# Kernel optimization log

Measured on AMD Instinct MI355X. Metric: run time of the kernel, lower is better.

## Reference

```python
import jax, jax.numpy as jnp
import numpy as np

T = 2048        # tokens
HID = 4096      # hidden_size
H = 32          # num attention heads
KV = 8          # num key/value heads (GQA)
D = HID // H    # head_dim = 128
THETA = 10000.0


def setup_inputs() -> dict:
    key = jax.random.key(0)
    k1, k2, k3 = jax.random.split(key, 3)
    hidden_states = jax.random.normal(k1, (T, HID), jnp.float32)
    positions = jnp.arange(T, dtype=jnp.int32)
    Wqkv = jax.random.normal(k2, ((H + 2 * KV) * D, HID), jnp.float32) * 0.02
    Wo = jax.random.normal(k3, (HID, H * D), jnp.float32) * 0.02
    return {"hidden_states": hidden_states, "positions": positions,
            "Wqkv": Wqkv, "Wo": Wo}


def _rope(positions, x):
    """Neox-style rotary embedding. x: [T, h, D], positions: [T]."""
    half = D // 2
    inv_freq = 1.0 / (THETA ** (jnp.arange(half, dtype=jnp.float32) / half))
    ang = positions.astype(jnp.float32)[:, None] * inv_freq      # [T, half]
    cos = jnp.cos(ang)[:, None, :]                                # [T, 1, half]
    sin = jnp.sin(ang)[:, None, :]
    x1, x2 = x[..., :half], x[..., half:]
    return jnp.concatenate([x1 * cos - x2 * sin, x2 * cos + x1 * sin], axis=-1)


def reference(hidden_states, positions, Wqkv, Wo):
    # fused QKV projection (no bias)
    qkv = hidden_states @ Wqkv.T                                  # [T, (H+2KV)*D]
    q, k, v = jnp.split(qkv, [H * D, H * D + KV * D], axis=1)
    q = q.reshape(T, H, D)
    k = k.reshape(T, KV, D)
    v = v.reshape(T, KV, D)
    # RoPE on q and k
    q = _rope(positions, q)
    k = _rope(positions, k)
    # GQA: expand kv heads to match q heads
    g = H // KV
    k = jnp.repeat(k, g, axis=1)                                  # [T, H, D]
    v = jnp.repeat(v, g, axis=1)
    # causal attention (flash-attention math)
    scores = jnp.einsum('thd,shd->hts', q, k) * (D ** -0.5)       # [H, T, T]
    causal = jnp.tril(jnp.ones((T, T), dtype=bool))
    scores = jnp.where(causal[None], scores, jnp.float32(-1e30))
    probs = jax.nn.softmax(scores, axis=-1)
    attn = jnp.einsum('hts,shd->thd', probs, v).reshape(T, H * D)
    # output projection
    return attn @ Wo.T
```

## Files before the change

### kernel.cpp

```cpp
#include <hip/hip_runtime.h>
#include <stdint.h>

#define T_SEQ 2048
#define HIDDEN 4096
#define NHEAD 32
#define NKV 8
#define HDIM 128
#define QKVN 6144

typedef __bf16 bf16x8 __attribute__((ext_vector_type(8)));
typedef float f32x4 __attribute__((ext_vector_type(4)));
typedef unsigned short u16;
typedef u16 u16x8 __attribute__((ext_vector_type(8)));
typedef u16 u16x4 __attribute__((ext_vector_type(4)));

__device__ __forceinline__ u16 f2bf(float f) {
  uint32_t u = __builtin_bit_cast(uint32_t, f);
  u = (u + 0x7fffu + ((u >> 16) & 1u)) >> 16;
  return (u16)u;
}
__device__ __forceinline__ float bf2f(u16 h) {
  uint32_t u = ((uint32_t)h) << 16;
  return __builtin_bit_cast(float, u);
}

__device__ __forceinline__ void gload16(const void* g, void* l) {
  __builtin_amdgcn_global_load_lds(
      (__attribute__((address_space(1))) void*)(uintptr_t)g,
      (__attribute__((address_space(3))) void*)(uintptr_t)l, 16, 0, 0);
}

__global__ void cvt_f32_bf16(const float* __restrict__ in, u16* __restrict__ out, int n) {
  int i = (blockIdx.x * blockDim.x + threadIdx.x) * 4;
  int stride = gridDim.x * blockDim.x * 4;
  for (; i < n; i += stride) {
    float4 v = *(const float4*)(in + i);
    u16x4 o;
    o.x = f2bf(v.x); o.y = f2bf(v.y); o.z = f2bf(v.z); o.w = f2bf(v.w);
    *(u16x4*)(out + i) = o;
  }
}

__global__ void rope_kernel(u16* __restrict__ qkv, const int* __restrict__ pos) {
  int idx = blockIdx.x * blockDim.x + threadIdx.x;
  if (idx >= T_SEQ * 40 * 64) return;
  int i = idx & 63;
  int head = (idx >> 6) % 40;
  int t = idx / (40 * 64);
  int base = head < NHEAD ? head * HDIM : NHEAD * HDIM + (head - NHEAD) * HDIM;
  float p = (float)pos[t];
  float inv_freq = exp2f(-(float)i * (13.287712379549449f / 64.0f));
  float ang = p * inv_freq;
  float s, c;
  sincosf(ang, &s, &c);
  u16* p1 = qkv + (size_t)t * QKVN + base + i;
  u16* p2 = p1 + 64;
  float x1 = bf2f(*p1), x2 = bf2f(*p2);
  *p1 = f2bf(x1 * c - x2 * s);
  *p2 = f2bf(x2 * c + x1 * s);
}

__device__ __forceinline__ void storeC(float* p, float v) { *p = v; }
__device__ __forceinline__ void storeC(u16* p, float v) { *p = f2bf(v); }
__device__ __forceinline__ f32x4 mfma16(bf16x8 a, bf16x8 b, f32x4 c) {
  return __builtin_amdgcn_mfma_f32_16x16x32_bf16(a, b, c, 0, 0, 0);
}

template <typename OutT, bool FUSED>
__global__ void __launch_bounds__(512, 2)
gemm256(const u16* __restrict__ A, const u16* __restrict__ B,
        OutT* __restrict__ C0, OutT* __restrict__ C1,
        int N, int K, int NT, int sliceBlocks, int nGemm,
        int nbx, int rw, int rh,
        const float* __restrict__ cvt_in, u16* __restrict__ cvt_out, int cvt_n4) {
  if (FUSED && (int)blockIdx.x >= nGemm) {
    int i = (blockIdx.x - nGemm) * blockDim.x + threadIdx.x;
    int stride = (gridDim.x - nGemm) * blockDim.x;
    for (; i < cvt_n4; i += stride) {
      float4 v = ((const float4*)cvt_in)[i];
      u16x4 o;
      o.x = f2bf(v.x); o.y = f2bf(v.y); o.z = f2bf(v.z); o.w = f2bf(v.w);
      ((u16x4*)cvt_out)[i] = o;
    }
    return;
  }

  __shared__ u16 As_[2][256 * 64];
  __shared__ u16 Bs_[2][256 * 64];

  const int tid = threadIdx.x;
  const int lane = tid & 63;
  const int w = tid >> 6;
  const int wr = w >> 2, wc = w & 3;
  const int l15 = lane & 15, lg = lane >> 4;

  const int bid = blockIdx.x;
  const int slice = bid / sliceBlocks;
  const int wi = bid % sliceBlocks;
  const int k0 = slice * (NT << 6);
  OutT* __restrict__ C = slice ? C1 : C0;

  const int c8 = wi & 7, i8 = wi >> 3;
  const int rpr = nbx / rw;
  const int by = (c8 / rpr) * rh + (i8 % rh);
  const int bx = (c8 % rpr) * rw + (i8 / rh);
  const int bm = by * 256, bn = bx * 256;

  const int u_lo = w * 64 + lane, u_hi = u_lo + 512;
  const int r0 = u_lo >> 3, s0 = (u_lo & 7) ^ (r0 & 7);
  const int r1 = u_hi >> 3, s1 = (u_hi & 7) ^ (r1 & 7);
  const u16* a0s0 = A + (size_t)(bm + r0) * K + k0 + s0 * 8;
  const u16* a0s1 = A + (size_t)(bm + r1) * K + k0 + s1 * 8;
  const u16* a1s0 = A + (size_t)(bm + 128 + r0) * K + k0 + s0 * 8;
  const u16* a1s1 = A + (size_t)(bm + 128 + r1) * K + k0 + s1 * 8;
  const u16* b0s0 = B + (size_t)(bn + r0) * K + k0 + s0 * 8;
  const u16* b0s1 = B + (size_t)(bn + r1) * K + k0 + s1 * 8;
  const u16* b1s0 = B + (size_t)(bn + 128 + r0) * K + k0 + s0 * 8;
  const u16* b1s1 = B + (size_t)(bn + 128 + r1) * K + k0 + s1 * 8;

  const int ax = l15 & 7;
  const int sl0 = (lg ^ ax) * 8;
  const int sl1 = ((4 + lg) ^ ax) * 8;
  const int a_row = (wr * 128 + l15) * 64;
  const int b_row = (wc * 64 + l15) * 64;

  f32x4 acc[8][4] = {};
  bf16x8 bfr[4][2];

#define BARRIER() asm volatile("s_barrier" ::: "memory")
#define WAITBAR(n_) asm volatile("s_waitcnt vmcnt(" #n_ ")\n\ts_barrier" ::: "memory")
#define STAGE_HALF(p0_, p1_, dst_, t_)                                         \
  {                                                                            \
    gload16((p0_) + (size_t)(t_) * 64, (dst_) + (size_t)w * 512);              \
    gload16((p1_) + (size_t)(t_) * 64, (dst_) + 4096 + (size_t)w * 512);       \
  }

  STAGE_HALF(a0s0, a0s1, &As_[0][0], 0);
  STAGE_HALF(a1s0, a1s1, &As_[0][8192], 0);
  STAGE_HALF(b0s0, b0s1, &Bs_[0][0], 0);
  STAGE_HALF(b1s0, b1s1, &Bs_[0][8192], 0);
  STAGE_HALF(b0s0, b0s1, &Bs_[1][0], 1);
  STAGE_HALF(b1s0, b1s1, &Bs_[1][8192], 1);
  WAITBAR(4);

  for (int v = 0; v < NT; ++v) {
    const int cur = v & 1, alt = cur ^ 1;
    const u16* Ac = &As_[cur][0];
    const u16* Bc = &Bs_[cur][0];
    const bool s1ok = (v + 1) < NT, s2ok = (v + 2) < NT;

#define MFMA_QUAD(p_, A0_, A1_, A2_, A3_)                                      \
    __builtin_amdgcn_s_setprio(1);                                             \
    _Pragma("unroll") for (int ni = 0; ni < 4; ++ni) {                         \
      acc[2 * (p_)][ni] = mfma16(A0_, bfr[ni][0], acc[2 * (p_)][ni]);          \
      acc[2 * (p_)][ni] = mfma16(A1_, bfr[ni][1], acc[2 * (p_)][ni]);          \
      acc[2 * (p_) + 1][ni] = mfma16(A2_, bfr[ni][0], acc[2 * (p_) + 1][ni]);  \
      acc[2 * (p_) + 1][ni] = mfma16(A3_, bfr[ni][1], acc[2 * (p_) + 1][ni]);  \
    }                                                                          \
    __builtin_amdgcn_s_setprio(0);

    {
#pragma unroll
      for (int ni = 0; ni < 4; ++ni) {
        bfr[ni][0] = *(const bf16x8*)&Bc[b_row + ni * 1024 + sl0];
        bfr[ni][1] = *(const bf16x8*)&Bc[b_row + ni * 1024 + sl1];
      }
      bf16x8 f0 = *(const bf16x8*)&Ac[a_row + 0 * 1024 + sl0];
      bf16x8 f1 = *(const bf16x8*)&Ac[a_row + 0 * 1024 + sl1];
      bf16x8 f2 = *(const bf16x8*)&Ac[a_row + 1 * 1024 + sl0];
      bf16x8 f3 = *(const bf16x8*)&Ac[a_row + 1 * 1024 + sl1];
      if (s1ok) STAGE_HALF(a0s0, a0s1, &As_[alt][0], v + 1);
      BARRIER();
      MFMA_QUAD(0, f0, f1, f2, f3);
      BARRIER();
    }
    {
      bf16x8 f0 = *(const bf16x8*)&Ac[a_row + 2 * 1024 + sl0];
      bf16x8 f1 = *(const bf16x8*)&Ac[a_row + 2 * 1024 + sl1];
      bf16x8 f2 = *(const bf16x8*)&Ac[a_row + 3 * 1024 + sl0];
      bf16x8 f3 = *(const bf16x8*)&Ac[a_row + 3 * 1024 + sl1];
      if (s1ok) STAGE_HALF(a1s0, a1s1, &As_[alt][8192], v + 1);
      if (s2ok) STAGE_HALF(b0s0, b0s1, &Bs_[cur][0], v + 2);
      BARRIER();
      MFMA_QUAD(1, f0, f1, f2, f3);
      BARRIER();
    }
    {
      bf16x8 f0 = *(const bf16x8*)&Ac[a_row + 4 * 1024 + sl0];
      bf16x8 f1 = *(const bf16x8*)&Ac[a_row + 4 * 1024 + sl1];
      bf16x8 f2 = *(const bf16x8*)&Ac[a_row + 5 * 1024 + sl0];
      bf16x8 f3 = *(const bf16x8*)&Ac[a_row + 5 * 1024 + sl1];
      if (s2ok) STAGE_HALF(b1s0, b1s1, &Bs_[cur][8192], v + 2);
      BARRIER();
      MFMA_QUAD(2, f0, f1, f2, f3);
      BARRIER();
    }
    {
      bf16x8 f0 = *(const bf16x8*)&Ac[a_row + 6 * 1024 + sl0];
      bf16x8 f1 = *(const bf16x8*)&Ac[a_row + 6 * 1024 + sl1];
      bf16x8 f2 = *(const bf16x8*)&Ac[a_row + 7 * 1024 + sl0];
      bf16x8 f3 = *(const bf16x8*)&Ac[a_row + 7 * 1024 + sl1];
      BARRIER();
      MFMA_QUAD(3, f0, f1, f2, f3);
      if (s2ok) { WAITBAR(4); } else { WAITBAR(0); }
    }
#undef MFMA_QUAD
  }

#pragma unroll
  for (int mi = 0; mi < 8; ++mi)
#pragma unroll
    for (int ni = 0; ni < 4; ++ni)
#pragma unroll
      for (int r = 0; r < 4; ++r) {
        int row = bm + wr * 128 + mi * 16 + lg * 4 + r;
        int col = bn + wc * 64 + ni * 16 + l15;
        storeC(&C[(size_t)row * N + col], acc[mi][ni][r]);
      }
#undef STAGE_HALF
#undef WAITBAR
#undef BARRIER
}

__global__ void reduce_add(float* __restrict__ out, const float* __restrict__ part, int n4) {
  int i = blockIdx.x * blockDim.x + threadIdx.x;
  int stride = gridDim.x * blockDim.x;
  for (; i < n4; i += stride) {
    float4 a = ((const float4*)out)[i];
    float4 b = ((const float4*)part)[i];
    a.x += b.x; a.y += b.y; a.z += b.z; a.w += b.w;
    ((float4*)out)[i] = a;
  }
}

__global__ void __launch_bounds__(256)
attn_kernel(const u16* __restrict__ qkv, u16* __restrict__ out) {
  __shared__ u16 Ksh[2][64 * 128];
  __shared__ u16 Vsh[2][128 * 64];
  __shared__ u16 Psh[4][16 * 64];

  const int tid = threadIdx.x;
  const int lane = tid & 63;
  const int w = tid >> 6;
  const int l15 = lane & 15, lg = lane >> 4;

  const int bid = blockIdx.x;
  const int kvh = bid & 7;
  const int hg = (bid >> 3) & 3;
  const int qi = 31 - (bid >> 5);
  const int h = kvh * 4 + hg;
  const int q0 = qi * 64;
  const int nt = qi + 1;

  const u16* Kg = qkv + NHEAD * HDIM + kvh * HDIM;
  const u16* Vg = qkv + (NHEAD + NKV) * HDIM + kvh * HDIM;

  bf16x8 qa[4];
  {
    const u16* qrow = qkv + (size_t)(q0 + w * 16 + l15) * QKVN + h * HDIM + lg * 8;
#pragma unroll
    for (int ks = 0; ks < 4; ++ks) qa[ks] = *(const bf16x8*)(qrow + ks * 32);
  }

  f32x4 acc_o[8] = {};
  float m[4], lsum[4];
#pragma unroll
  for (int r = 0; r < 4; ++r) { m[r] = -1e30f; lsum[r] = 0.f; }

  const float scale = 0.088388347648318447f;

#define STAGE_K(kv0, p)                                                        \
  {                                                                            \
    _Pragma("unroll") for (int rnd = 0; rnd < 4; ++rnd) {                      \
      int cc = rnd * 256 + tid;                                                \
      int krow = cc >> 4, kslot = cc & 15;                                     \
      gload16(Kg + (size_t)((kv0) + krow) * QKVN + (kslot ^ (krow & 7)) * 8,   \
              &Ksh[p][(rnd * 256 + w * 64) * 8]);                              \
    }                                                                          \
  }
#define LOAD_V(kv0, vr)                                                        \
  {                                                                            \
    _Pragma("unroll") for (int rnd = 0; rnd < 4; ++rnd) {                      \
      int cc = rnd * 256 + tid;                                                \
      int vrow = cc >> 4, d0 = (cc & 15) * 8;                                  \
      vr[rnd] = *(const u16x8*)(Vg + (size_t)((kv0) + vrow) * QKVN + d0);      \
    }                                                                          \
  }
#define WRITE_V(vr, p)                                                         \
  {                                                                            \
    _Pragma("unroll") for (int rnd = 0; rnd < 4; ++rnd) {                      \
      int cc = rnd * 256 + tid;                                                \
      int vrow = cc >> 4, d0 = (cc & 15) * 8;                                  \
      _Pragma("unroll") for (int j = 0; j < 8; ++j) {                          \
        int d = d0 + j;                                                        \
        Vsh[p][d * 64 + (((vrow >> 3) ^ (d & 7) ^ ((d >> 3) & 7)) * 8) +       \
               (vrow & 7)] = vr[rnd][j];                                       \
      }                                                                        \
    }                                                                          \
  }

  u16x8 vreg[4];
  STAGE_K(0, 0);
  LOAD_V(0, vreg);
  WRITE_V(vreg, 0);
  __syncthreads();

  for (int t = 0; t < nt; ++t) {
    const int p = t & 1;
    const int kv0 = t * 64;
    const bool more = (t + 1 < nt);
    u16x8 vnext[4];
    if (more) {
      STAGE_K(kv0 + 64, p ^ 1);
      LOAD_V(kv0 + 64, vnext);
    }

    f32x4 s[4] = {};
#pragma unroll
    for (int ks = 0; ks < 4; ++ks) {
#pragma unroll
      for (int n = 0; n < 4; ++n) {
        int row16 = n * 16 + l15;
        bf16x8 kf = *(const bf16x8*)&Ksh[p][row16 * 128 +
                                            (((ks * 4 + lg) ^ (row16 & 7)) * 8)];
        s[n] = __builtin_amdgcn_mfma_f32_16x16x32_bf16(qa[ks], kf, s[n], 0, 0, 0);
      }
    }

    const bool diag = (t == nt - 1);
    float alpha[4];
#pragma unroll
    for (int r = 0; r < 4; ++r) {
      int tq = q0 + w * 16 + lg * 4 + r;
      float mx = -1e30f;
#pragma unroll
      for (int n = 0; n < 4; ++n) {
        float v = s[n][r] * scale;
        if (diag && (kv0 + n * 16 + l15) > tq) v = -1e30f;
        s[n][r] = v;
        mx = fmaxf(mx, v);
      }
#pragma unroll
      for (int msk = 1; msk < 16; msk <<= 1) mx = fmaxf(mx, __shfl_xor(mx, msk, 64));
      float mn = fmaxf(m[r], mx);
      alpha[r] = __expf(m[r] - mn);
      m[r] = mn;
      float ps = 0.f;
#pragma unroll
      for (int n = 0; n < 4; ++n) {
        float pv = __expf(s[n][r] - mn);
        s[n][r] = pv;
        ps += pv;
      }
#pragma unroll
      for (int msk = 1; msk < 16; msk <<= 1) ps += __shfl_xor(ps, msk, 64);
      lsum[r] = lsum[r] * alpha[r] + ps;
      int prow = lg * 4 + r;
#pragma unroll
      for (int n = 0; n < 4; ++n)
        Psh[w][prow * 64 + (((n * 2 + (l15 >> 3)) ^ (prow & 7)) * 8) + (l15 & 7)] =
            f2bf(s[n][r]);
    }
#pragma unroll
    for (int f = 0; f < 8; ++f)
#pragma unroll
      for (int r = 0; r < 4; ++r) acc_o[f][r] *= alpha[r];

#pragma unroll
    for (int ks = 0; ks < 2; ++ks) {
      bf16x8 pa = *(const bf16x8*)&Psh[w][l15 * 64 + (((ks * 4 + lg) ^ (l15 & 7)) * 8)];
#pragma unroll
      for (int nd = 0; nd < 8; ++nd) {
        int d = nd * 16 + l15;
        bf16x8 bv = *(const bf16x8*)&Vsh[p][d * 64 +
                        (((ks * 4 + lg) ^ (d & 7) ^ ((d >> 3) & 7)) * 8)];
        acc_o[nd] = __builtin_amdgcn_mfma_f32_16x16x32_bf16(pa, bv, acc_o[nd], 0, 0, 0);
      }
    }

    if (more) WRITE_V(vnext, p ^ 1);
    __syncthreads();
  }

#pragma unroll
  for (int nd = 0; nd < 8; ++nd)
#pragma unroll
    for (int r = 0; r < 4; ++r) {
      int row = q0 + w * 16 + lg * 4 + r;
      int col = h * HDIM + nd * 16 + l15;
      out[(size_t)row * (NHEAD * HDIM) + col] = f2bf(acc_o[nd][r] / lsum[r]);
    }
#undef STAGE_K
#undef LOAD_V
#undef WRITE_V
}

extern "C" void kernel_launch(void* const* d_in, const int* in_sizes, int n_in,
                              void* d_out, int out_size, void* d_ws, size_t ws_size,
                              hipStream_t stream) {
  const float* hs   = (const float*)d_in[0];
  const int*   pos  = (const int*)d_in[1];
  const float* wqkv = (const float*)d_in[2];
  const float* wo   = (const float*)d_in[3];
  float* out = (float*)d_out;
  uint8_t* ws = (uint8_t*)d_ws;

  if (ws_size < 142606336u) return;
  u16* hs_bf   = (u16*)(ws + 0);
  u16* wqkv_bf = (u16*)(ws + 16777216u);
  u16* wo_bf   = (u16*)(ws + 67108864u);
  u16* qkv_bf  = (u16*)(ws + 100663296u);
  u16* attn_bf = (u16*)(ws + 125829120u);
  float* part  = (float*)(ws + 16777216u);

  cvt_f32_bf16<<<2048, 256, 0, stream>>>(hs, hs_bf, T_SEQ * HIDDEN);
  cvt_f32_bf16<<<2048, 256, 0, stream>>>(wqkv, wqkv_bf, QKVN * HIDDEN);

  gemm256<u16, true><<<256, 512, 0, stream>>>(
      hs_bf, wqkv_bf, qkv_bf, qkv_bf, QKVN, HIDDEN, 64,
      192, 192, 24, 3, 8, wo, wo_bf, (HIDDEN * HIDDEN) / 4);

  rope_kernel<<<(T_SEQ * 40 * 64) / 256, 256, 0, stream>>>(qkv_bf, pos);

  attn_kernel<<<1024, 256, 0, stream>>>(qkv_bf, attn_bf);

  gemm256<float, false><<<256, 512, 0, stream>>>(
      attn_bf, wo_bf, out, part, HIDDEN, HIDDEN, 32,
      128, 256, 16, 2, 8, nullptr, nullptr, 0);

  reduce_add<<<2048, 256, 0, stream>>>(out, part, (T_SEQ * HIDDEN) / 4);
}
```

Baseline: 353.9 us.

## Enlarge attention query tile and pre-transpose V for async LDS staging

Adds a separate kernel that transposes V into a [kvh][d][T] buffer so the attention kernel can stage V tiles with direct async global-to-LDS loads instead of register round-trips and scalar scattered LDS writes. The attention block now covers 128 query rows (32 per wave, two MFMA row tiles), so each K/V fragment read from LDS feeds twice as many MFMAs. Blocks are ordered to pair long and short causal rows, and fully masked tiles are skipped per wave. This costs an extra transpose launch and a V round trip through memory, halves the grid to 512 blocks, and raises register pressure.

```diff
diff --git a/kernel.cpp b/kernel.cpp
--- a/kernel.cpp
+++ b/kernel.cpp
@@ -60,6 +60,35 @@
   *p2 = f2bf(x2 * c + x1 * s);
 }
 
+__global__ void vt_kernel(const u16* __restrict__ qkv, u16* __restrict__ vt) {
+  __shared__ u16 tile[64][64];
+  const int tid = threadIdx.x;
+  const int tb = blockIdx.x;
+  const int kvh = blockIdx.y >> 1;
+  const int d0 = (blockIdx.y & 1) * 64;
+  const u16* src = qkv + (size_t)(NHEAD + NKV) * HDIM + kvh * HDIM + d0;
+#pragma unroll
+  for (int g = 0; g < 2; ++g) {
+    int u = g * 256 + tid;
+    int t = u >> 3, ds = u & 7;
+    u16x8 v = *(const u16x8*)(src + (size_t)(tb * 64 + t) * QKVN + ds * 8);
+#pragma unroll
+    for (int j = 0; j < 8; ++j) {
+      int d = ds * 8 + j;
+      tile[d][(((t >> 3) ^ (d & 7)) * 8) + (t & 7)] = v[j];
+    }
+  }
+  __syncthreads();
+  u16* dst = vt + ((size_t)kvh * HDIM + d0) * T_SEQ + tb * 64;
+#pragma unroll
+  for (int g = 0; g < 2; ++g) {
+    int u = g * 256 + tid;
+    int d = u >> 3, s = u & 7;
+    u16x8 v = *(const u16x8*)&tile[d][(s ^ (d & 7)) * 8];
+    *(u16x8*)(dst + (size_t)d * T_SEQ + s * 8) = v;
+  }
+}
+
 __device__ __forceinline__ void storeC(float* p, float v) { *p = v; }
 __device__ __forceinline__ void storeC(u16* p, float v) { *p = f2bf(v); }
 __device__ __forceinline__ f32x4 mfma16(bf16x8 a, bf16x8 b, f32x4 c) {
@@ -233,11 +262,12 @@
   }
 }
 
-__global__ void __launch_bounds__(256)
-attn_kernel(const u16* __restrict__ qkv, u16* __restrict__ out) {
+__global__ void __launch_bounds__(256, 2)
+attn_kernel(const u16* __restrict__ qkv, const u16* __restrict__ vt,
+            u16* __restrict__ out) {
   __shared__ u16 Ksh[2][64 * 128];
   __shared__ u16 Vsh[2][128 * 64];
-  __shared__ u16 Psh[4][16 * 64];
+  __shared__ u16 Psh[4][32 * 64];
 
   const int tid = threadIdx.x;
   const int lane = tid & 63;
@@ -245,27 +275,31 @@
   const int l15 = lane & 15, lg = lane >> 4;
 
   const int bid = blockIdx.x;
-  const int kvh = bid & 7;
-  const int hg = (bid >> 3) & 3;
-  const int qi = 31 - (bid >> 5);
+  const int u8 = bid & 255, sfl = bid >> 8;
+  const int kvh = u8 & 7;
+  const int hg = (u8 >> 3) & 3;
+  const int x = (u8 >> 5) & 7;
+  const int qi = sfl ? x : (15 - x);
   const int h = kvh * 4 + hg;
-  const int q0 = qi * 64;
-  const int nt = qi + 1;
+  const int q0 = qi * 128;
+  const int nt = 2 * qi + 2;
+  const int wrow = q0 + w * 32;
 
   const u16* Kg = qkv + NHEAD * HDIM + kvh * HDIM;
-  const u16* Vg = qkv + (NHEAD + NKV) * HDIM + kvh * HDIM;
-
-  bf16x8 qa[4];
-  {
-    const u16* qrow = qkv + (size_t)(q0 + w * 16 + l15) * QKVN + h * HDIM + lg * 8;
-#pragma unroll
-    for (int ks = 0; ks < 4; ++ks) qa[ks] = *(const bf16x8*)(qrow + ks * 32);
-  }
-
-  f32x4 acc_o[8] = {};
-  float m[4], lsum[4];
-#pragma unroll
-  for (int r = 0; r < 4; ++r) { m[r] = -1e30f; lsum[r] = 0.f; }
+  const u16* Vg = vt + (size_t)kvh * HDIM * T_SEQ;
+
+  bf16x8 qa[2][4];
+#pragma unroll
+  for (int mi = 0; mi < 2; ++mi) {
+    const u16* qrow = qkv + (size_t)(wrow + mi * 16 + l15) * QKVN + h * HDIM + lg * 8;
+#pragma unroll
+    for (int ks = 0; ks < 4; ++ks) qa[mi][ks] = *(const bf16x8*)(qrow + ks * 32);
+  }
+
+  f32x4 acc_o[2][8] = {};
+  float m[8], lsum[8];
+#pragma unroll
+  for (int r = 0; r < 8; ++r) { m[r] = -1e30f; lsum[r] = 0.f; }
 
   const float scale = 0.088388347648318447f;
 
@@ -278,121 +312,116 @@
               &Ksh[p][(rnd * 256 + w * 64) * 8]);                              \
     }                                                                          \
   }
-#define LOAD_V(kv0, vr)                                                        \
+#define STAGE_V(kv0, p)                                                        \
   {                                                                            \
     _Pragma("unroll") for (int rnd = 0; rnd < 4; ++rnd) {                      \
       int cc = rnd * 256 + tid;                                                \
-      int vrow = cc >> 4, d0 = (cc & 15) * 8;                                  \
-      vr[rnd] = *(const u16x8*)(Vg + (size_t)((kv0) + vrow) * QKVN + d0);      \
+      int vrow = cc >> 3, ps = cc & 7;                                         \
+      gload16(Vg + (size_t)vrow * T_SEQ + (kv0) + ((ps ^ (vrow & 7)) * 8),     \
+              &Vsh[p][(rnd * 256 + w * 64) * 8]);                              \
     }                                                                          \
   }
-#define WRITE_V(vr, p)                                                         \
-  {                                                                            \
-    _Pragma("unroll") for (int rnd = 0; rnd < 4; ++rnd) {                      \
-      int cc = rnd * 256 + tid;                                                \
-      int vrow = cc >> 4, d0 = (cc & 15) * 8;                                  \
-      _Pragma("unroll") for (int j = 0; j < 8; ++j) {                          \
-        int d = d0 + j;                                                        \
-        Vsh[p][d * 64 + (((vrow >> 3) ^ (d & 7) ^ ((d >> 3) & 7)) * 8) +       \
-               (vrow & 7)] = vr[rnd][j];                                       \
-      }                                                                        \
-    }                                                                          \
-  }
-
-  u16x8 vreg[4];
+
   STAGE_K(0, 0);
-  LOAD_V(0, vreg);
-  WRITE_V(vreg, 0);
+  STAGE_V(0, 0);
   __syncthreads();
 
   for (int t = 0; t < nt; ++t) {
     const int p = t & 1;
     const int kv0 = t * 64;
     const bool more = (t + 1 < nt);
-    u16x8 vnext[4];
     if (more) {
       STAGE_K(kv0 + 64, p ^ 1);
-      LOAD_V(kv0 + 64, vnext);
-    }
-
-    f32x4 s[4] = {};
-#pragma unroll
-    for (int ks = 0; ks < 4; ++ks) {
-#pragma unroll
-      for (int n = 0; n < 4; ++n) {
-        int row16 = n * 16 + l15;
-        bf16x8 kf = *(const bf16x8*)&Ksh[p][row16 * 128 +
-                                            (((ks * 4 + lg) ^ (row16 & 7)) * 8)];
-        s[n] = __builtin_amdgcn_mfma_f32_16x16x32_bf16(qa[ks], kf, s[n], 0, 0, 0);
+      STAGE_V(kv0 + 64, p ^ 1);
+    }
+
+    if (kv0 <= wrow + 31) {
+      f32x4 s[2][4] = {};
+#pragma unroll
+      for (int ks = 0; ks < 4; ++ks) {
+#pragma unroll
+        for (int n = 0; n < 4; ++n) {
+          int row16 = n * 16 + l15;
+          bf16x8 kf = *(const bf16x8*)&Ksh[p][row16 * 128 +
+                                              (((ks * 4 + lg) ^ (row16 & 7)) * 8)];
+          s[0][n] = mfma16(qa[0][ks], kf, s[0][n]);
+          s[1][n] = mfma16(qa[1][ks], kf, s[1][n]);
+        }
       }
-    }
-
-    const bool diag = (t == nt - 1);
-    float alpha[4];
-#pragma unroll
-    for (int r = 0; r < 4; ++r) {
-      int tq = q0 + w * 16 + lg * 4 + r;
-      float mx = -1e30f;
-#pragma unroll
-      for (int n = 0; n < 4; ++n) {
-        float v = s[n][r] * scale;
-        if (diag && (kv0 + n * 16 + l15) > tq) v = -1e30f;
-        s[n][r] = v;
-        mx = fmaxf(mx, v);
+
+      const bool diag = (kv0 + 63 > wrow);
+      float alpha[8];
+#pragma unroll
+      for (int mi = 0; mi < 2; ++mi)
+#pragma unroll
+        for (int r = 0; r < 4; ++r) {
+          int ri = mi * 4 + r;
+          int tq = wrow + mi * 16 + lg * 4 + r;
+          float mx = -1e30f;
+#pragma unroll
+          for (int n = 0; n < 4; ++n) {
+            float v = s[mi][n][r] * scale;
+            if (diag && (kv0 + n * 16 + l15) > tq) v = -1e30f;
+            s[mi][n][r] = v;
+            mx = fmaxf(mx, v);
+          }
+#pragma unroll
+          for (int msk = 1; msk < 16; msk <<= 1) mx = fmaxf(mx, __shfl_xor(mx, msk, 64));
+          float mn = fmaxf(m[ri], mx);
+          alpha[ri] = __expf(m[ri] - mn);
+          m[ri] = mn;
+          float ps = 0.f;
+#pragma unroll
+          for (int n = 0; n < 4; ++n) {
+            float pv = __expf(s[mi][n][r] - mn);
+            s[mi][n][r] = pv;
+            ps += pv;
+          }
+#pragma unroll
+          for (int msk = 1; msk < 16; msk <<= 1) ps += __shfl_xor(ps, msk, 64);
+          lsum[ri] = lsum[ri] * alpha[ri] + ps;
+          int prow = mi * 16 + lg * 4 + r;
+#pragma unroll
+          for (int n = 0; n < 4; ++n)
+            Psh[w][prow * 64 + (((n * 2 + (l15 >> 3)) ^ (prow & 7)) * 8) + (l15 & 7)] =
+                f2bf(s[mi][n][r]);
+        }
+#pragma unroll
+      for (int mi = 0; mi < 2; ++mi)
+#pragma unroll
+        for (int f = 0; f < 8; ++f)
+#pragma unroll
+          for (int r = 0; r < 4; ++r) acc_o[mi][f][r] *= alpha[mi * 4 + r];
+
+#pragma unroll
+      for (int ks = 0; ks < 2; ++ks) {
+        bf16x8 pa0 = *(const bf16x8*)&Psh[w][l15 * 64 + (((ks * 4 + lg) ^ (l15 & 7)) * 8)];
+        bf16x8 pa1 = *(const bf16x8*)&Psh[w][(16 + l15) * 64 + (((ks * 4 + lg) ^ (l15 & 7)) * 8)];
+#pragma unroll
+        for (int nd = 0; nd < 8; ++nd) {
+          int d = nd * 16 + l15;
+          bf16x8 bv = *(const bf16x8*)&Vsh[p][d * 64 + (((ks * 4 + lg) ^ (d & 7)) * 8)];
+          acc_o[0][nd] = mfma16(pa0, bv, acc_o[0][nd]);
+          acc_o[1][nd] = mfma16(pa1, bv, acc_o[1][nd]);
+        }
       }
-#pragma unroll
-      for (int msk = 1; msk < 16; msk <<= 1) mx = fmaxf(mx, __shfl_xor(mx, msk, 64));
-      float mn = fmaxf(m[r], mx);
-      alpha[r] = __expf(m[r] - mn);
-      m[r] = mn;
-      float ps = 0.f;
-#pragma unroll
-      for (int n = 0; n < 4; ++n) {
-        float pv = __expf(s[n][r] - mn);
-        s[n][r] = pv;
-        ps += pv;
+    }
+
+    __syncthreads();
+  }
+
+#pragma unroll
+  for (int mi = 0; mi < 2; ++mi)
+#pragma unroll
+    for (int nd = 0; nd < 8; ++nd)
+#pragma unroll
+      for (int r = 0; r < 4; ++r) {
+        int row = wrow + mi * 16 + lg * 4 + r;
+        int col = h * HDIM + nd * 16 + l15;
+        out[(size_t)row * (NHEAD * HDIM) + col] = f2bf(acc_o[mi][nd][r] / lsum[mi * 4 + r]);
       }
-#pragma unroll
-      for (int msk = 1; msk < 16; msk <<= 1) ps += __shfl_xor(ps, msk, 64);
-      lsum[r] = lsum[r] * alpha[r] + ps;
-      int prow = lg * 4 + r;
-#pragma unroll
-      for (int n = 0; n < 4; ++n)
-        Psh[w][prow * 64 + (((n * 2 + (l15 >> 3)) ^ (prow & 7)) * 8) + (l15 & 7)] =
-            f2bf(s[n][r]);
-    }
-#pragma unroll
-    for (int f = 0; f < 8; ++f)
-#pragma unroll
-      for (int r = 0; r < 4; ++r) acc_o[f][r] *= alpha[r];
-
-#pragma unroll
-    for (int ks = 0; ks < 2; ++ks) {
-      bf16x8 pa = *(const bf16x8*)&Psh[w][l15 * 64 + (((ks * 4 + lg) ^ (l15 & 7)) * 8)];
-#pragma unroll
-      for (int nd = 0; nd < 8; ++nd) {
-        int d = nd * 16 + l15;
-        bf16x8 bv = *(const bf16x8*)&Vsh[p][d * 64 +
-                        (((ks * 4 + lg) ^ (d & 7) ^ ((d >> 3) & 7)) * 8)];
-        acc_o[nd] = __builtin_amdgcn_mfma_f32_16x16x32_bf16(pa, bv, acc_o[nd], 0, 0, 0);
-      }
-    }
-
-    if (more) WRITE_V(vnext, p ^ 1);
-    __syncthreads();
-  }
-
-#pragma unroll
-  for (int nd = 0; nd < 8; ++nd)
-#pragma unroll
-    for (int r = 0; r < 4; ++r) {
-      int row = q0 + w * 16 + lg * 4 + r;
-      int col = h * HDIM + nd * 16 + l15;
-      out[(size_t)row * (NHEAD * HDIM) + col] = f2bf(acc_o[nd][r] / lsum[r]);
-    }
 #undef STAGE_K
-#undef LOAD_V
-#undef WRITE_V
+#undef STAGE_V
 }
 
 extern "C" void kernel_launch(void* const* d_in, const int* in_sizes, int n_in,
@@ -412,6 +441,7 @@
   u16* qkv_bf  = (u16*)(ws + 100663296u);
   u16* attn_bf = (u16*)(ws + 125829120u);
   float* part  = (float*)(ws + 16777216u);
+  u16* vt_buf  = (u16*)(ws + 0);
 
   cvt_f32_bf16<<<2048, 256, 0, stream>>>(hs, hs_bf, T_SEQ * HIDDEN);
   cvt_f32_bf16<<<2048, 256, 0, stream>>>(wqkv, wqkv_bf, QKVN * HIDDEN);
@@ -422,7 +452,9 @@
 
   rope_kernel<<<(T_SEQ * 40 * 64) / 256, 256, 0, stream>>>(qkv_bf, pos);
 
-  attn_kernel<<<1024, 256, 0, stream>>>(qkv_bf, attn_bf);
+  vt_kernel<<<dim3(32, 16), 256, 0, stream>>>(qkv_bf, vt_buf);
+
+  attn_kernel<<<512, 256, 0, stream>>>(qkv_bf, vt_buf, attn_bf);
 
   gemm256<float, false><<<256, 512, 0, stream>>>(
       attn_bf, wo_bf, out, part, HIDDEN, HIDDEN, 32,
```

After: 366.5 us. +3.6%, slower.
